# Optimization experiments

Hardware: AMD Instinct MI355X
Metric: run time of the kernel (lower is better)

## Reference

```python
import jax, jax.numpy as jnp
import numpy as np

N_POINTS = 2_000_000
GRID = 256  # voxel grid resolution (D=H=W), production-scale stand-in for source's 128


def setup_inputs() -> dict:
    key = jax.random.key(0)
    k1, k2, k3 = jax.random.split(key, 3)
    coords = jax.random.uniform(k1, (N_POINTS, 3), dtype=jnp.float32,
                                minval=-0.95, maxval=0.95)
    registration_pred = jax.random.normal(k2, (N_POINTS, 3), dtype=jnp.float32) * 0.02
    registration_gt = jax.random.normal(k3, (N_POINTS, 3), dtype=jnp.float32) * 0.02
    return {"registration_pred": registration_pred,
            "registration_gt": registration_gt,
            "coords": coords}


def _splat(pts, size):
    """Trilinear scatter (adjoint of F.grid_sample, align_corners=False,
    zero padding). pts: [N,3] normalized coords in (x,y,z) order mapping to
    (W,H,D). Splats weight 1 per point. Returns [D,H,W] volume."""
    D = H = W = size
    # grid_sample align_corners=False unnormalization: p = ((g+1)*size - 1)/2
    x = ((pts[:, 0] + 1.0) * W - 1.0) * 0.5
    y = ((pts[:, 1] + 1.0) * H - 1.0) * 0.5
    z = ((pts[:, 2] + 1.0) * D - 1.0) * 0.5
    x0f, y0f, z0f = jnp.floor(x), jnp.floor(y), jnp.floor(z)
    fx, fy, fz = x - x0f, y - y0f, z - z0f  # fractional offsets
    x0, y0, z0 = x0f.astype(jnp.int32), y0f.astype(jnp.int32), z0f.astype(jnp.int32)
    vol = jnp.zeros(D * H * W, dtype=pts.dtype)
    for dz in (0, 1):
        wz = fz if dz else (1.0 - fz)
        for dy in (0, 1):
            wy = fy if dy else (1.0 - fy)
            for dx in (0, 1):
                wx = fx if dx else (1.0 - fx)
                xi, yi, zi = x0 + dx, y0 + dy, z0 + dz
                valid = ((xi >= 0) & (xi < W) & (yi >= 0) & (yi < H)
                         & (zi >= 0) & (zi < D))
                w = jnp.where(valid, wx * wy * wz, 0.0)
                idx = jnp.where(valid, (zi * H + yi) * W + xi, 0)
                vol = vol.at[idx].add(w)
    return vol.reshape(D, H, W)


def reference(registration_pred, registration_gt, coords):
    pred_vol = _splat(coords + registration_pred, GRID)
    gt_vol = _splat(coords + registration_gt, GRID)
    # HuberLoss(reduction='sum', delta=1.0)
    d = pred_vol - gt_vol
    ad = jnp.abs(d)
    return jnp.sum(jnp.where(ad <= 1.0, 0.5 * d * d, ad - 0.5))
```

## Files before the change

### kernel.cpp

```cpp
#include <hip/hip_runtime.h>

#define GRID_RES 256
#define NCELLS 1024
#define NB 1024
#define BCAP 6144
#define CCAP 6144
#define NPT 2

#define W_SCALE 2097152.0f
#define INV_W (1.0f / 2097152.0f)
#define L_SCALE 512.0f
#define INV_L (1.0f / 512.0f)

struct CEv { unsigned w0, w1q, xyz; };

__device__ __forceinline__ CEv make_cev(float px, float py, float pz,
                                        unsigned sign) {
    float x = ((px + 1.0f) * (float)GRID_RES - 1.0f) * 0.5f;
    float y = ((py + 1.0f) * (float)GRID_RES - 1.0f) * 0.5f;
    float z = ((pz + 1.0f) * (float)GRID_RES - 1.0f) * 0.5f;
    float xf = floorf(x), yf = floorf(y), zf = floorf(z);
    int x0 = (int)xf, y0 = (int)yf, z0 = (int)zf;
    unsigned qx = (unsigned)((x - xf) * 65535.0f + 0.5f);
    unsigned qy = (unsigned)((y - yf) * 65535.0f + 0.5f);
    unsigned qz = (unsigned)((z - zf) * 16383.0f + 0.5f);
    bool valid = (x0 >= -1) & (x0 <= 255) & (y0 >= -1) & (y0 <= 255) &
                 (z0 >= -1) & (z0 <= 255);
    CEv e;
    e.w0 = qx | (qy << 16);
    e.w1q = qz | (sign << 31);
    e.xyz = valid ? ((unsigned)(x0 + 1) | ((unsigned)(y0 + 1) << 10) |
                     ((unsigned)(z0 + 1) << 20) | (1u << 30))
                  : 0u;
    return e;
}

__device__ __forceinline__ bool ev_flat(const CEv& e, unsigned& cell0,
                                        unsigned& w1base, bool& bx, bool& by,
                                        bool& bz) {
    if (!(e.xyz & (1u << 30))) return false;
    int x0 = (int)(e.xyz & 1023u) - 1;
    int y0 = (int)((e.xyz >> 10) & 1023u) - 1;
    int z0 = (int)((e.xyz >> 20) & 1023u) - 1;
    int xlo = (x0 >= 0) ? (x0 >> 5) : 0;
    int ylo = (y0 >= 0) ? (y0 >> 5) : 0;
    int zlo = (z0 >= 0) ? (z0 >> 4) : 0;
    bx = ((x0 & 31) == 31) & ((unsigned)x0 < 255u);
    by = ((y0 & 31) == 31) & ((unsigned)y0 < 255u);
    bz = ((z0 & 15) == 15) & ((unsigned)z0 < 255u);
    cell0 = ((unsigned)zlo << 6) | ((unsigned)ylo << 3) | (unsigned)xlo;
    unsigned lx0 = (unsigned)(x0 - (xlo << 5) + 1);
    unsigned ly0 = (unsigned)(y0 - (ylo << 5) + 1);
    unsigned lz0 = (unsigned)(z0 - (zlo << 4) + 1);
    w1base = e.w1q | (lx0 << 14) | (ly0 << 20) | (lz0 << 26);
    return true;
}

__global__ void init_kernel(unsigned* __restrict__ gCursor,
                            int* __restrict__ lossAcc,
                            unsigned* __restrict__ doneCnt) {
    int t = threadIdx.x;
    gCursor[t] = 0;
    if (t == 0) { lossAcc[0] = 0; doneCnt[0] = 0; }
}

__global__ __launch_bounds__(1024) void bin_kernel(
    const float* __restrict__ pred, const float* __restrict__ gt,
    const float* __restrict__ coords, unsigned* __restrict__ gCursor,
    uint2* __restrict__ payload, int n) {
    __shared__ unsigned h[NCELLS];
    __shared__ unsigned gAdj[NCELLS];
    __shared__ unsigned short itemCell[BCAP];
    __shared__ unsigned wtot[16];
    __shared__ unsigned totalS;
    __shared__ uint2 pl[BCAP];
    int b = blockIdx.x;
    int t = threadIdx.x;
    h[t] = 0;
    __syncthreads();

    int chunk = (n + NB - 1) / NB;
    int start = b * chunk;
    int end = min(start + chunk, n);
    const float3* c3 = (const float3*)coords;
    const float3* p3 = (const float3*)pred;
    const float3* g3 = (const float3*)gt;

    CEv ev[2 * NPT];
#pragma unroll
    for (int k = 0; k < NPT; ++k) {
        int i = start + t + (k << 10);
        if (i < end) {
            float3 c = c3[i];
            float3 p = p3[i];
            float3 g = g3[i];
            ev[2 * k] = make_cev(c.x + p.x, c.y + p.y, c.z + p.z, 0u);
            ev[2 * k + 1] = make_cev(c.x + g.x, c.y + g.y, c.z + g.z, 1u);
        } else {
            ev[2 * k].xyz = 0;
            ev[2 * k + 1].xyz = 0;
        }
    }

#pragma unroll
    for (int k = 0; k < 2 * NPT; ++k) {
        unsigned cell0, w1base;
        bool bx, by, bz;
        if (ev_flat(ev[k], cell0, w1base, bx, by, bz)) {
#pragma unroll
            for (int r = 0; r < 8; ++r) {
                const int DX = r & 1, DY = (r >> 1) & 1, DZ = r >> 2;
                bool go = (DX ? bx : true) & (DY ? by : true) & (DZ ? bz : true);
                if (go) atomicAdd(&h[cell0 + DX + 8 * DY + 64 * DZ], 1u);
            }
        }
    }
    __syncthreads();

    unsigned x = h[t];
    unsigned xp = x + (x & 1u);
    unsigned incl = xp;
    int lane = t & 63, wid = t >> 6;
#pragma unroll
    for (int off = 1; off < 64; off <<= 1) {
        unsigned y = __shfl_up(incl, off, 64);
        if (lane >= off) incl += y;
    }
    if (lane == 63) wtot[wid] = incl;
    __syncthreads();
    if (t == 0) {
        unsigned r = 0;
#pragma unroll
        for (int w = 0; w < 16; ++w) { unsigned v = wtot[w]; wtot[w] = r; r += v; }
        totalS = r;
    }
    __syncthreads();
    unsigned offE = incl - xp + wtot[wid];
    h[t] = offE;

    if ((x & 1u) && (offE + x) < (unsigned)BCAP) {
        pl[offE + x] = make_uint2(0u, 0u);
        itemCell[offE + x] = (unsigned short)t;
    }

    unsigned gdst = atomicAdd(&gCursor[t], xp);
    gAdj[t] = (unsigned)t * (unsigned)CCAP + gdst - offE;
    __syncthreads();

#pragma unroll
    for (int k = 0; k < 2 * NPT; ++k) {
        unsigned cell0, w1base;
        bool bx, by, bz;
        if (ev_flat(ev[k], cell0, w1base, bx, by, bz)) {
            unsigned w0 = ev[k].w0;
#pragma unroll
            for (int r = 0; r < 8; ++r) {
                const int DX = r & 1, DY = (r >> 1) & 1, DZ = r >> 2;
                bool go = (DX ? bx : true) & (DY ? by : true) & (DZ ? bz : true);
                if (go) {
                    unsigned cell = cell0 + DX + 8 * DY + 64 * DZ;
                    unsigned w1 = w1base - (((unsigned)DX << 19) +
                                            ((unsigned)DY << 25) +
                                            ((unsigned)DZ << 30));
                    unsigned slot = atomicAdd(&h[cell], 1u);
                    if (slot < (unsigned)BCAP) {
                        pl[slot] = make_uint2(w0, w1);
                        itemCell[slot] = (unsigned short)cell;
                    }
                }
            }
        }
    }
    __syncthreads();

    unsigned tot = min(totalS, (unsigned)BCAP);
    unsigned np = tot >> 1;
    const uint4* plq4 = (const uint4*)pl;
    uint4* pay4 = (uint4*)payload;
    for (unsigned j = t; j < np; j += 1024) {
        unsigned cell = itemCell[2 * j];
        unsigned e = gAdj[cell] + 2u * j;
        if (e + 2u <= (cell + 1u) * (unsigned)CCAP) pay4[e >> 1] = plq4[j];
    }
}

__device__ __forceinline__ void accum_item(uint2 p, int* v) {
    float fx = (float)(p.x & 0xFFFFu) * (1.0f / 65535.0f);
    float fy = (float)(p.x >> 16) * (1.0f / 65535.0f);
    float fz = (float)(p.y & 0x3FFFu) * (1.0f / 16383.0f);
    int lx = (int)((p.y >> 14) & 63u);
    int ly = (int)((p.y >> 20) & 63u);
    int lz = (int)((p.y >> 26) & 31u);
    float s = (p.y >> 31) ? -W_SCALE : W_SCALE;
    float wxs[2] = {1.0f - fx, fx};
    float wys[2] = {1.0f - fy, fy};
    float wzs[2] = {1.0f - fz, fz};
    int xb = lx - 1, yb = ly - 1, zb = lz - 1;
#pragma unroll
    for (int dz = 0; dz < 2; ++dz) {
        int rz = zb + dz;
        if ((unsigned)rz > 15u) continue;
        float wz = s * wzs[dz];
#pragma unroll
        for (int dy = 0; dy < 2; ++dy) {
            int ry = yb + dy;
            if ((unsigned)ry > 31u) continue;
            float wyz = wz * wys[dy];
#pragma unroll
            for (int dx = 0; dx < 2; ++dx) {
                int rx = xb + dx;
                if ((unsigned)rx > 31u) continue;
                int iw = __float2int_rn(wyz * wxs[dx]);
                atomicAdd(&v[(rz << 10) | (ry << 5) | rx], iw);
            }
        }
    }
}

__global__ __launch_bounds__(1024) void accum_kernel(
    const uint2* __restrict__ payload, const unsigned* __restrict__ gCursor,
    int* __restrict__ lossAcc, unsigned* __restrict__ doneCnt,
    float* __restrict__ out) {
    __shared__ int4 v4s[4096];
    __shared__ float wsum[16];
    int* v = (int*)v4s;
    int c = blockIdx.x;
    int t = threadIdx.x;
    unsigned cnt = min(gCursor[c], (unsigned)CCAP) & ~1u;
    int4 z; z.x = 0; z.y = 0; z.z = 0; z.w = 0;
#pragma unroll
    for (int j = 0; j < 4; ++j) v4s[t + (j << 10)] = z;
    __syncthreads();

    const uint4* p4 = (const uint4*)(payload + (size_t)c * CCAP);
    unsigned n2 = cnt >> 1;
#pragma unroll 2
    for (unsigned i = t; i < n2; i += 1024) {
        uint4 q = p4[i];
        uint2 pa; pa.x = q.x; pa.y = q.y;
        uint2 pb; pb.x = q.z; pb.y = q.w;
        accum_item(pa, v);
        accum_item(pb, v);
    }
    __syncthreads();

    int lane = t & 63, wid = t >> 6;
    float acc = 0.0f;
#pragma unroll
    for (int j = 0; j < 4; ++j) {
        int4 q = v4s[t + (j << 10)];
        {
            float d = (float)q.x * INV_W;
            float ad = fabsf(d);
            acc += (ad <= 1.0f) ? 0.5f * d * d : ad - 0.5f;
        }
        {
            float d = (float)q.y * INV_W;
            float ad = fabsf(d);
            acc += (ad <= 1.0f) ? 0.5f * d * d : ad - 0.5f;
        }
        {
            float d = (float)q.z * INV_W;
            float ad = fabsf(d);
            acc += (ad <= 1.0f) ? 0.5f * d * d : ad - 0.5f;
        }
        {
            float d = (float)q.w * INV_W;
            float ad = fabsf(d);
            acc += (ad <= 1.0f) ? 0.5f * d * d : ad - 0.5f;
        }
    }
#pragma unroll
    for (int o = 32; o > 0; o >>= 1) acc += __shfl_down(acc, o, 64);
    if (lane == 0) wsum[wid] = acc;
    __syncthreads();
    if (t == 0) {
        float tsum = 0.0f;
#pragma unroll
        for (int w = 0; w < 16; ++w) tsum += wsum[w];
        atomicAdd(lossAcc, __float2int_rn(tsum * L_SCALE));
        __threadfence();
        unsigned done = atomicAdd(doneCnt, 1u);
        if (done == (unsigned)(NCELLS - 1)) {
            __threadfence();
            int lv = atomicAdd(lossAcc, 0);
            out[0] = (float)lv * INV_L;
        }
    }
}

extern "C" void kernel_launch(void* const* d_in, const int* in_sizes, int n_in,
                              void* d_out, int out_size, void* d_ws, size_t ws_size,
                              hipStream_t stream) {
    const float* reg_pred = (const float*)d_in[0];
    const float* reg_gt   = (const float*)d_in[1];
    const float* coords   = (const float*)d_in[2];
    float* out = (float*)d_out;

    char* ws = (char*)d_ws;
    int* lossAcc = (int*)ws;
    unsigned* doneCnt = (unsigned*)(ws + 64);
    unsigned* gCursor = (unsigned*)(ws + 256);
    uint2* payload = (uint2*)(ws + 256 + 4096);

    int n = in_sizes[0] / 3;

    init_kernel<<<1, 1024, 0, stream>>>(gCursor, lossAcc, doneCnt);
    bin_kernel<<<NB, 1024, 0, stream>>>(reg_pred, reg_gt, coords, gCursor,
                                        payload, n);
    accum_kernel<<<NCELLS, 1024, 0, stream>>>(payload, gCursor, lossAcc,
                                              doneCnt, out);
}
```

Before: 165.3 us.

## Fuse init, bin and accumulate kernels into one cooperative grid-synced kernel

```diff
diff --git a/kernel.cpp b/kernel.cpp
--- a/kernel.cpp
+++ b/kernel.cpp
@@ -1,8 +1,12 @@
 #include <hip/hip_runtime.h>
+#include <hip/hip_cooperative_groups.h>
+
+namespace cg = cooperative_groups;
 
 #define GRID_RES 256
 #define NCELLS 1024
 #define NB 1024
+#define BCAP2 5632
 #define BCAP 6144
 #define CCAP 6144
 #define NPT 2
@@ -56,6 +60,247 @@
     return true;
 }
 
+__device__ __forceinline__ void accum_item(uint2 p, int* v) {
+    float fx = (float)(p.x & 0xFFFFu) * (1.0f / 65535.0f);
+    float fy = (float)(p.x >> 16) * (1.0f / 65535.0f);
+    float fz = (float)(p.y & 0x3FFFu) * (1.0f / 16383.0f);
+    int lx = (int)((p.y >> 14) & 63u);
+    int ly = (int)((p.y >> 20) & 63u);
+    int lz = (int)((p.y >> 26) & 31u);
+    float s = (p.y >> 31) ? -W_SCALE : W_SCALE;
+    float wxs[2] = {1.0f - fx, fx};
+    float wys[2] = {1.0f - fy, fy};
+    float wzs[2] = {1.0f - fz, fz};
+    int xb = lx - 1, yb = ly - 1, zb = lz - 1;
+#pragma unroll
+    for (int dz = 0; dz < 2; ++dz) {
+        int rz = zb + dz;
+        if ((unsigned)rz > 15u) continue;
+        float wz = s * wzs[dz];
+#pragma unroll
+        for (int dy = 0; dy < 2; ++dy) {
+            int ry = yb + dy;
+            if ((unsigned)ry > 31u) continue;
+            float wyz = wz * wys[dy];
+#pragma unroll
+            for (int dx = 0; dx < 2; ++dx) {
+                int rx = xb + dx;
+                if ((unsigned)rx > 31u) continue;
+                int iw = __float2int_rn(wyz * wxs[dx]);
+                atomicAdd(&v[(rz << 10) | (ry << 5) | rx], iw);
+            }
+        }
+    }
+}
+
+struct BinS2 {
+    uint2 pl[BCAP2];
+    unsigned h[NCELLS];
+    unsigned gAdj[NCELLS];
+    unsigned short itemCell[BCAP2];
+    unsigned wtot[16];
+    unsigned totalS;
+};
+#define SMEM2 65536
+
+__global__ __launch_bounds__(1024, 8) void fused_kernel(
+    const float* __restrict__ pred, const float* __restrict__ gt,
+    const float* __restrict__ coords, unsigned* __restrict__ gCursor,
+    uint2* __restrict__ payload, int* __restrict__ lossAcc,
+    unsigned* __restrict__ doneCnt, float* __restrict__ out, int n) {
+    __shared__ __align__(16) char smem[SMEM2];
+    BinS2& S = *(BinS2*)smem;
+    int4* v4s = (int4*)smem;
+    int* v = (int*)smem;
+    cg::grid_group grid = cg::this_grid();
+    int b = blockIdx.x;
+    int G = gridDim.x;
+    int t = threadIdx.x;
+    int lane = t & 63, wid = t >> 6;
+
+    if (b == 0) {
+        gCursor[t] = 0;
+        if (t == 0) { lossAcc[0] = 0; doneCnt[0] = 0; }
+    }
+    grid.sync();
+
+    int chunk = (n + NB - 1) / NB;
+    const float3* c3 = (const float3*)coords;
+    const float3* p3 = (const float3*)pred;
+    const float3* g3 = (const float3*)gt;
+
+    for (int blk = b; blk < NB; blk += G) {
+        S.h[t] = 0;
+        __syncthreads();
+
+        int start = blk * chunk;
+        int end = min(start + chunk, n);
+        CEv ev[2 * NPT];
+#pragma unroll
+        for (int k = 0; k < NPT; ++k) {
+            int i = start + t + (k << 10);
+            if (i < end) {
+                float3 c = c3[i];
+                float3 p = p3[i];
+                float3 g = g3[i];
+                ev[2 * k] = make_cev(c.x + p.x, c.y + p.y, c.z + p.z, 0u);
+                ev[2 * k + 1] = make_cev(c.x + g.x, c.y + g.y, c.z + g.z, 1u);
+            } else {
+                ev[2 * k].xyz = 0;
+                ev[2 * k + 1].xyz = 0;
+            }
+        }
+
+#pragma unroll
+        for (int k = 0; k < 2 * NPT; ++k) {
+            unsigned cell0, w1base;
+            bool bx, by, bz;
+            if (ev_flat(ev[k], cell0, w1base, bx, by, bz)) {
+#pragma unroll
+                for (int q = 0; q < 8; ++q) {
+                    const int DX = q & 1, DY = (q >> 1) & 1, DZ = q >> 2;
+                    bool go = (DX ? bx : true) & (DY ? by : true) &
+                              (DZ ? bz : true);
+                    if (go) atomicAdd(&S.h[cell0 + DX + 8 * DY + 64 * DZ], 1u);
+                }
+            }
+        }
+        __syncthreads();
+
+        unsigned x = S.h[t];
+        unsigned xp = x + (x & 1u);
+        unsigned incl = xp;
+#pragma unroll
+        for (int off = 1; off < 64; off <<= 1) {
+            unsigned y = __shfl_up(incl, off, 64);
+            if (lane >= off) incl += y;
+        }
+        if (lane == 63) S.wtot[wid] = incl;
+        __syncthreads();
+        if (t == 0) {
+            unsigned rr = 0;
+#pragma unroll
+            for (int w = 0; w < 16; ++w) {
+                unsigned q = S.wtot[w];
+                S.wtot[w] = rr;
+                rr += q;
+            }
+            S.totalS = rr;
+        }
+        __syncthreads();
+        unsigned offE = incl - xp + S.wtot[wid];
+        S.h[t] = offE;
+
+        if ((x & 1u) && (offE + x) < (unsigned)BCAP2) {
+            S.pl[offE + x] = make_uint2(0u, 0u);
+            S.itemCell[offE + x] = (unsigned short)t;
+        }
+
+        unsigned gdst = atomicAdd(&gCursor[t], xp);
+        S.gAdj[t] = (unsigned)t * (unsigned)CCAP + gdst - offE;
+        __syncthreads();
+
+#pragma unroll
+        for (int k = 0; k < 2 * NPT; ++k) {
+            unsigned cell0, w1base;
+            bool bx, by, bz;
+            if (ev_flat(ev[k], cell0, w1base, bx, by, bz)) {
+                unsigned w0 = ev[k].w0;
+#pragma unroll
+                for (int q = 0; q < 8; ++q) {
+                    const int DX = q & 1, DY = (q >> 1) & 1, DZ = q >> 2;
+                    bool go = (DX ? bx : true) & (DY ? by : true) &
+                              (DZ ? bz : true);
+                    if (go) {
+                        unsigned cell = cell0 + DX + 8 * DY + 64 * DZ;
+                        unsigned w1 = w1base - (((unsigned)DX << 19) +
+                                                ((unsigned)DY << 25) +
+                                                ((unsigned)DZ << 30));
+                        unsigned slot = atomicAdd(&S.h[cell], 1u);
+                        if (slot < (unsigned)BCAP2) {
+                            S.pl[slot] = make_uint2(w0, w1);
+                            S.itemCell[slot] = (unsigned short)cell;
+                        }
+                    }
+                }
+            }
+        }
+        __syncthreads();
+
+        unsigned tot = min(S.totalS, (unsigned)BCAP2);
+        unsigned np = tot >> 1;
+        const uint4* plq4 = (const uint4*)S.pl;
+        uint4* pay4 = (uint4*)payload;
+        for (unsigned j = t; j < np; j += 1024) {
+            unsigned cell = S.itemCell[2 * j];
+            unsigned e = S.gAdj[cell] + 2u * j;
+            if (e + 2u <= (cell + 1u) * (unsigned)CCAP) pay4[e >> 1] = plq4[j];
+        }
+        __syncthreads();
+    }
+    grid.sync();
+
+    for (int c = b; c < NCELLS; c += G) {
+        unsigned cnt = min(gCursor[c], (unsigned)CCAP) & ~1u;
+        int4 z; z.x = 0; z.y = 0; z.z = 0; z.w = 0;
+#pragma unroll
+        for (int j = 0; j < 4; ++j) v4s[t + (j << 10)] = z;
+        __syncthreads();
+
+        const uint4* p4 = (const uint4*)(payload + (size_t)c * CCAP);
+        unsigned n2 = cnt >> 1;
+#pragma unroll 2
+        for (unsigned i = t; i < n2; i += 1024) {
+            uint4 q = p4[i];
+            uint2 pa; pa.x = q.x; pa.y = q.y;
+            uint2 pb; pb.x = q.z; pb.y = q.w;
+            accum_item(pa, v);
+            accum_item(pb, v);
+        }
+        __syncthreads();
+
+        float acc = 0.0f;
+#pragma unroll
+        for (int j = 0; j < 4; ++j) {
+            int4 q = v4s[t + (j << 10)];
+            {
+                float d = (float)q.x * INV_W;
+                float ad = fabsf(d);
+                acc += (ad <= 1.0f) ? 0.5f * d * d : ad - 0.5f;
+            }
+            {
+                float d = (float)q.y * INV_W;
+                float ad = fabsf(d);
+                acc += (ad <= 1.0f) ? 0.5f * d * d : ad - 0.5f;
+            }
+            {
+                float d = (float)q.z * INV_W;
+                float ad = fabsf(d);
+                acc += (ad <= 1.0f) ? 0.5f * d * d : ad - 0.5f;
+            }
+            {
+                float d = (float)q.w * INV_W;
+                float ad = fabsf(d);
+                acc += (ad <= 1.0f) ? 0.5f * d * d : ad - 0.5f;
+            }
+        }
+#pragma unroll
+        for (int o = 32; o > 0; o >>= 1) acc += __shfl_down(acc, o, 64);
+        if (lane == 0) atomicAdd(lossAcc, __float2int_rn(acc * L_SCALE));
+        __syncthreads();
+    }
+
+    if (t == 0) {
+        __threadfence();
+        unsigned done = atomicAdd(doneCnt, 1u);
+        if (done == (unsigned)(G - 1)) {
+            __threadfence();
+            int lv = atomicAdd(lossAcc, 0);
+            out[0] = (float)lv * INV_L;
+        }
+    }
+}
+
 __global__ void init_kernel(unsigned* __restrict__ gCursor,
                             int* __restrict__ lossAcc,
                             unsigned* __restrict__ doneCnt) {
@@ -108,8 +353,8 @@
         bool bx, by, bz;
         if (ev_flat(ev[k], cell0, w1base, bx, by, bz)) {
 #pragma unroll
-            for (int r = 0; r < 8; ++r) {
-                const int DX = r & 1, DY = (r >> 1) & 1, DZ = r >> 2;
+            for (int q = 0; q < 8; ++q) {
+                const int DX = q & 1, DY = (q >> 1) & 1, DZ = q >> 2;
                 bool go = (DX ? bx : true) & (DY ? by : true) & (DZ ? bz : true);
                 if (go) atomicAdd(&h[cell0 + DX + 8 * DY + 64 * DZ], 1u);
             }
@@ -131,7 +376,7 @@
     if (t == 0) {
         unsigned r = 0;
 #pragma unroll
-        for (int w = 0; w < 16; ++w) { unsigned v = wtot[w]; wtot[w] = r; r += v; }
+        for (int w = 0; w < 16; ++w) { unsigned q = wtot[w]; wtot[w] = r; r += q; }
         totalS = r;
     }
     __syncthreads();
@@ -154,8 +399,8 @@
         if (ev_flat(ev[k], cell0, w1base, bx, by, bz)) {
             unsigned w0 = ev[k].w0;
 #pragma unroll
-            for (int r = 0; r < 8; ++r) {
-                const int DX = r & 1, DY = (r >> 1) & 1, DZ = r >> 2;
+            for (int q = 0; q < 8; ++q) {
+                const int DX = q & 1, DY = (q >> 1) & 1, DZ = q >> 2;
                 bool go = (DX ? bx : true) & (DY ? by : true) & (DZ ? bz : true);
                 if (go) {
                     unsigned cell = cell0 + DX + 8 * DY + 64 * DZ;
@@ -184,39 +429,6 @@
     }
 }
 
-__device__ __forceinline__ void accum_item(uint2 p, int* v) {
-    float fx = (float)(p.x & 0xFFFFu) * (1.0f / 65535.0f);
-    float fy = (float)(p.x >> 16) * (1.0f / 65535.0f);
-    float fz = (float)(p.y & 0x3FFFu) * (1.0f / 16383.0f);
-    int lx = (int)((p.y >> 14) & 63u);
-    int ly = (int)((p.y >> 20) & 63u);
-    int lz = (int)((p.y >> 26) & 31u);
-    float s = (p.y >> 31) ? -W_SCALE : W_SCALE;
-    float wxs[2] = {1.0f - fx, fx};
-    float wys[2] = {1.0f - fy, fy};
-    float wzs[2] = {1.0f - fz, fz};
-    int xb = lx - 1, yb = ly - 1, zb = lz - 1;
-#pragma unroll
-    for (int dz = 0; dz < 2; ++dz) {
-        int rz = zb + dz;
-        if ((unsigned)rz > 15u) continue;
-        float wz = s * wzs[dz];
-#pragma unroll
-        for (int dy = 0; dy < 2; ++dy) {
-            int ry = yb + dy;
-            if ((unsigned)ry > 31u) continue;
-            float wyz = wz * wys[dy];
-#pragma unroll
-            for (int dx = 0; dx < 2; ++dx) {
-                int rx = xb + dx;
-                if ((unsigned)rx > 31u) continue;
-                int iw = __float2int_rn(wyz * wxs[dx]);
-                atomicAdd(&v[(rz << 10) | (ry << 5) | rx], iw);
-            }
-        }
-    }
-}
-
 __global__ __launch_bounds__(1024) void accum_kernel(
     const uint2* __restrict__ payload, const unsigned* __restrict__ gCursor,
     int* __restrict__ lossAcc, unsigned* __restrict__ doneCnt,
@@ -305,9 +517,26 @@
 
     int n = in_sizes[0] / 3;
 
-    init_kernel<<<1, 1024, 0, stream>>>(gCursor, lossAcc, doneCnt);
-    bin_kernel<<<NB, 1024, 0, stream>>>(reg_pred, reg_gt, coords, gCursor,
-                                        payload, n);
-    accum_kernel<<<NCELLS, 1024, 0, stream>>>(payload, gCursor, lossAcc,
-                                              doneCnt, out);
-}
+    bool coop_ok = false;
+    int maxB = 0;
+    hipError_t qerr = hipOccupancyMaxActiveBlocksPerMultiprocessor(
+        &maxB, (const void*)fused_kernel, 1024, 0);
+    if (qerr == hipSuccess && maxB >= 1) {
+        int nblk = maxB * 256;
+        if (nblk > 512) nblk = 512;
+        void* args[] = {(void*)&reg_pred, (void*)&reg_gt, (void*)&coords,
+                        (void*)&gCursor,  (void*)&payload, (void*)&lossAcc,
+                        (void*)&doneCnt,  (void*)&out,     (void*)&n};
+        hipError_t lerr = hipLaunchCooperativeKernel(
+            reinterpret_cast<void*>(&fused_kernel), dim3(nblk), dim3(1024),
+            args, 0, stream);
+        coop_ok = (lerr == hipSuccess);
+    }
+    if (!coop_ok) {
+        init_kernel<<<1, 1024, 0, stream>>>(gCursor, lossAcc, doneCnt);
+        bin_kernel<<<NB, 1024, 0, stream>>>(reg_pred, reg_gt, coords, gCursor,
+                                            payload, n);
+        accum_kernel<<<NCELLS, 1024, 0, stream>>>(payload, gCursor, lossAcc,
+                                                  doneCnt, out);
+    }
+}
```

Result: slower. 416.6 us (+152.1%).
